# Performance work log

Measured on AMD Instinct MI355X. Metric: run time of the kernel, lower is better.

The kernel has to match this reference:

```python
import jax, jax.numpy as jnp
import numpy as np

N, E, G = 50000, 800000, 128          # nodes, edges, graphs in batch
DF, DE, DT = 128, 256, 18             # dim_features, dim_embedding, dim_target
NUM_LAYERS = 4


def setup_inputs() -> dict:
    key = jax.random.key(0)
    ks = jax.random.split(key, 32)
    inp = {}
    inp["x"] = jax.random.normal(ks[0], (N, DF), jnp.float32)
    inp["edge_index"] = jax.random.randint(ks[1], (2, E), 0, N, dtype=jnp.int64)
    inp["batch"] = jnp.sort(jax.random.randint(ks[2], (N,), 0, G, dtype=jnp.int64))
    i = 3
    for l in range(NUM_LAYERS):
        din = DF if l == 0 else DE
        inp[f"Wl{l}"] = jax.random.normal(ks[i], (din, DE), jnp.float32) * (din ** -0.5); i += 1
        inp[f"bl{l}"] = jnp.zeros((DE,), jnp.float32)
        inp[f"Wr{l}"] = jax.random.normal(ks[i], (din, DE), jnp.float32) * (din ** -0.5); i += 1
        inp[f"Wm{l}"] = jax.random.normal(ks[i], (DE, DE), jnp.float32) * (DE ** -0.5); i += 1
        inp[f"bm{l}"] = jnp.zeros((DE,), jnp.float32)
    inp["fc1_W"] = jax.random.normal(ks[i], (NUM_LAYERS * DE, DE), jnp.float32) * ((NUM_LAYERS * DE) ** -0.5); i += 1
    inp["fc1_b"] = jnp.zeros((DE,), jnp.float32)
    inp["fc2_W"] = jax.random.normal(ks[i], (DE, DT), jnp.float32) * (DE ** -0.5); i += 1
    inp["fc2_b"] = jnp.zeros((DT,), jnp.float32)
    return inp


def _seg_max(v, idx, n):
    # scatter-max; empty segments -> 0 (PyG scatter 'max' convention)
    m = jax.ops.segment_max(v, idx, num_segments=n)
    return jnp.where(jnp.isfinite(m), m, 0.0)


def reference(x, edge_index, batch,
              Wl0, bl0, Wr0, Wm0, bm0,
              Wl1, bl1, Wr1, Wm1, bm1,
              Wl2, bl2, Wr2, Wm2, bm2,
              Wl3, bl3, Wr3, Wm3, bm3,
              fc1_W, fc1_b, fc2_W, fc2_b):
    src, dst = edge_index[0], edge_index[1]
    params = [(Wl0, bl0, Wr0, Wm0, bm0), (Wl1, bl1, Wr1, Wm1, bm1),
              (Wl2, bl2, Wr2, Wm2, bm2), (Wl3, bl3, Wr3, Wm3, bm3)]
    h = x
    outs = []
    for Wl, bl, Wr, Wm, bm in params:
        # SAGEConv(aggr='max'): lin_l(max_j x_j) + lin_r(x_i)
        agg = _seg_max(h[src], dst, h.shape[0])       # [N, din] gather + scatter-max
        h = agg @ Wl + bl + h @ Wr                    # [N, DE]
        h = jax.nn.relu(h @ Wm + bm)                  # fc_max + relu
        outs.append(h)
    hc = jnp.concatenate(outs, axis=1)                # [N, 4*DE]
    g = _seg_max(hc, batch, G)                        # global_max_pool -> [G, 4*DE]
    last_layer = jax.nn.relu(g @ fc1_W + fc1_b)       # [G, DE]
    out = last_layer @ fc2_W + fc2_b                  # [G, DT] (dropout = identity at eval)
    return jax.nn.log_softmax(out, axis=1), out, last_layer
```

## Files before the change

### kernel.cpp

```cpp
#include <hip/hip_runtime.h>
#include <stdint.h>

#define NN 50000
#define EE 800000
#define GG 128
#define DF 128
#define DE 256
#define NB 196

typedef unsigned short u16;
typedef __bf16 bf16x8 __attribute__((ext_vector_type(8)));
typedef float f32x4 __attribute__((ext_vector_type(4)));
typedef short s16x8 __attribute__((ext_vector_type(8)));

__device__ __forceinline__ float bf2f(u16 u) {
  union { unsigned int i; float f; } x; x.i = ((unsigned int)u) << 16; return x.f;
}
__device__ __forceinline__ u16 f2bf(float f) {
  union { float f; unsigned int i; } x; x.f = f;
  unsigned int i = x.i;
  return (u16)((i + 0x7fffu + ((i >> 16) & 1u)) >> 16);
}

__device__ __forceinline__ void async16(const void* g, void* l) {
  __builtin_amdgcn_global_load_lds(
      (const __attribute__((address_space(1))) void*)g,
      (__attribute__((address_space(3))) void*)l,
      16, 0, 0);
}

__device__ __forceinline__ s16x8 vmax8(s16x8 a, s16x8 b) {
  return __builtin_elementwise_max(a, b);
}

__global__ void detect_kernel(const u16* __restrict__ xr,
                              const unsigned* __restrict__ ei_words,
                              int* __restrict__ flags, int* __restrict__ bucket_cnt) {
  int tid = threadIdx.x;
  if (blockIdx.x == 1) {
    if (tid < NB) bucket_cnt[tid] = 0;
    return;
  }
  __shared__ int red[2];
  if (tid < 2) red[tid] = 0;
  __syncthreads();
  int found = 0;
  for (int it = 0; it < 32; it++) {
    int i = it * 256 + tid;
    u16 a = xr[2 * i], b = xr[2 * i + 1];
    if (((a >> 7) & 0xFFu) == 0xFFu) found = 1;
    if (((b >> 7) & 0xFFu) == 0xFFu) found = 1;
  }
  if (__ballot(found)) { if ((tid & 63) == 0) atomicOr(&red[0], 1); }
  int nz = 0;
  if (tid < 128) {
    for (int j = 0; j < 4; j++) {
      unsigned w = ei_words[2 * (tid * 4 + j) + 1];
      if (w != 0u) nz = 1;
    }
  }
  if (__ballot(nz)) { if ((tid & 63) == 0) atomicOr(&red[1], 1); }
  __syncthreads();
  if (tid == 0) { flags[0] = red[0]; flags[1] = red[1]; }
}

__device__ __forceinline__ u16 ldw(const void* p, int idx, int f) {
  return f ? f2bf(((const float*)p)[idx]) : ((const u16*)p)[idx];
}

struct ConvSeg { const void* src; u16* dst; int start_blk; int n; };

struct PrepArgs {
  ConvSeg s[12]; int nseg; int conv_blocks;
  const void* x; u16* acat_x; u16* xk;
  const void* ei; const void* batch;
  int* src32; int* dst32; int* batch32; int* bucket_cnt;
};

__global__ void prep_all(PrepArgs A, const int* __restrict__ flags) {
  int f = flags[0];
  int tid = threadIdx.x;
  int b = blockIdx.x;

  if (b < A.conv_blocks) {
    for (int i = 0; i < A.nseg; i++) {
      int nb = (A.s[i].n + 255) >> 8;
      if (b >= A.s[i].start_blk && b < A.s[i].start_blk + nb) {
        int idx = ((b - A.s[i].start_blk) << 8) + tid;
        if (idx < A.s[i].n) A.s[i].dst[idx] = ldw(A.s[i].src, idx, f);
        return;
      }
    }
    return;
  }
  b -= A.conv_blocks;

  if (b < 25000) {
    int i = b * 256 + tid;
    int node = i >> 7, d = i & 127;
    u16 v = ldw(A.x, i, f);
    A.acat_x[(long)node * 512 + d] = v;
    short s = (short)v;
    A.xk[i] = (u16)(s ^ ((s >> 15) & 0x7FFF));
    return;
  }
  b -= 25000;

  __shared__ int h[NB];
  if (tid < NB) h[tid] = 0;
  __syncthreads();
  int i64 = (flags[1] == 0);
  int e0 = b * 2048;
  for (int j = 0; j < 8; j++) {
    int i = e0 + j * 256 + tid;
    if (i < EE) {
      int s, d;
      if (i64) {
        s = (int)((const long long*)A.ei)[i];
        d = (int)((const long long*)A.ei)[EE + i];
      } else {
        s = ((const int*)A.ei)[i];
        d = ((const int*)A.ei)[EE + i];
      }
      s = min(max(s, 0), NN - 1);
      d = min(max(d, 0), NN - 1);
      A.src32[i] = s;
      A.dst32[i] = d;
      atomicAdd(&h[d >> 8], 1);
    }
    if (i < NN) {
      int bv = i64 ? (int)((const long long*)A.batch)[i] : ((const int*)A.batch)[i];
      A.batch32[i] = min(max(bv, 0), GG - 1);
    }
  }
  __syncthreads();
  if (tid < NB) atomicAdd(&A.bucket_cnt[tid], h[tid]);
}

struct TransArgs {
  const void* Wl[4]; const void* Wr[4]; const void* Wm[4]; const void* fc1W;
  u16* WcatT[4]; u16* WmT[4]; u16* fc1WT;
};

__global__ __launch_bounds__(256) void transpose_w(TransArgs T, const int* __restrict__ flags) {
  int f = flags[0];
  __shared__ u16 tile[64][65];
  int b = blockIdx.x;
  const void* src; u16* dst; int kt, ntile, Kd; int krow_off = 0;
  if (b < 16) {
    kt = b >> 2; ntile = b & 3; Kd = 256;
    if (kt * 64 < 128) { src = T.Wl[0]; } else { src = T.Wr[0]; krow_off = 128; }
    dst = T.WcatT[0];
  } else if (b < 112) {
    int l = 1 + (b - 16) / 32; int t = (b - 16) % 32;
    kt = t >> 2; ntile = t & 3; Kd = 512;
    if (kt * 64 < 256) { src = T.Wl[l]; } else { src = T.Wr[l]; krow_off = 256; }
    dst = T.WcatT[l];
  } else if (b < 176) {
    int l = (b - 112) / 16; int t = (b - 112) % 16;
    kt = t >> 2; ntile = t & 3; Kd = 256;
    src = T.Wm[l]; dst = T.WmT[l];
  } else {
    int t = b - 176;
    kt = t >> 2; ntile = t & 3; Kd = 1024;
    src = T.fc1W; dst = T.fc1WT;
  }
  int cj = threadIdx.x & 63, rp = threadIdx.x >> 6;
#pragma unroll 4
  for (int p = 0; p < 16; p++) {
    int krow = kt * 64 + p * 4 + rp;
    tile[p * 4 + rp][cj] = ldw(src, (krow - krow_off) * 256 + ntile * 64 + cj, f);
  }
  __syncthreads();
#pragma unroll 4
  for (int p = 0; p < 16; p++) {
    int nrow = ntile * 64 + p * 4 + rp;
    dst[(long)nrow * Kd + kt * 64 + cj] = tile[cj][p * 4 + rp];
  }
}

__global__ void bucket_scan(const int* __restrict__ bucket_cnt, int* __restrict__ bucket_base,
                            int* __restrict__ bucket_cur,
                            const int* __restrict__ batch, int* __restrict__ gs) {
  __shared__ int sh[256];
  int tid = threadIdx.x;
  int x = (tid < NB) ? bucket_cnt[tid] : 0;
  sh[tid] = x;
  __syncthreads();
  for (int off = 1; off < 256; off <<= 1) {
    int v = (tid >= off) ? sh[tid - off] : 0;
    __syncthreads();
    sh[tid] += v;
    __syncthreads();
  }
  if (tid < NB) { bucket_base[tid] = sh[tid] - x; bucket_cur[tid] = sh[tid] - x; }
  if (tid == 0) bucket_base[NB] = EE;
  if (tid <= GG) {
    int g = tid, lo = 0, hi = NN;
    while (lo < hi) { int mid = (lo + hi) >> 1; if (batch[mid] < g) lo = mid + 1; else hi = mid; }
    gs[g] = lo;
  }
}

__global__ __launch_bounds__(256) void bucket_pass1(
    const int* __restrict__ src32, const int* __restrict__ dst32,
    int* __restrict__ bucket_cur, unsigned* __restrict__ bucket_buf) {
  __shared__ int lcnt[NB];
  __shared__ int lbase[NB];
  int tid = threadIdx.x, b = blockIdx.x;
  if (tid < NB) lcnt[tid] = 0;
  __syncthreads();
  int e0 = b * 2048;
  int lofs[8]; unsigned pk[8]; int bk[8];
#pragma unroll
  for (int j = 0; j < 8; j++) {
    int i = e0 + j * 256 + tid;
    if (i < EE) {
      int s = src32[i], d = dst32[i];
      bk[j] = d >> 8;
      pk[j] = ((unsigned)s << 8) | (unsigned)(d & 255);
      lofs[j] = atomicAdd(&lcnt[bk[j]], 1);
    } else bk[j] = -1;
  }
  __syncthreads();
  if (tid < NB) lbase[tid] = atomicAdd(&bucket_cur[tid], lcnt[tid]);
  __syncthreads();
#pragma unroll
  for (int j = 0; j < 8; j++)
    if (bk[j] >= 0)
      bucket_buf[lbase[bk[j]] + lofs[j]] = pk[j];
}

__global__ __launch_bounds__(256) void bucket_pass2(
    const unsigned* __restrict__ bucket_buf, const int* __restrict__ bucket_base,
    int* __restrict__ col_src, int* __restrict__ row_ptr) {
  __shared__ int cnt[256];
  __shared__ int sh[256];
  __shared__ int cur[256];
  int tid = threadIdx.x, b = blockIdx.x;
  int ebase = bucket_base[b], eend = bucket_base[b + 1];
  cnt[tid] = 0;
  __syncthreads();
  for (int e = ebase + tid; e < eend; e += 256)
    atomicAdd(&cnt[bucket_buf[e] & 255u], 1);
  __syncthreads();
  int x = cnt[tid];
  sh[tid] = x;
  __syncthreads();
  for (int off = 1; off < 256; off <<= 1) {
    int v = (tid >= off) ? sh[tid - off] : 0;
    __syncthreads();
    sh[tid] += v;
    __syncthreads();
  }
  int node = b * 256 + tid;
  if (node < NN) row_ptr[node + 1] = ebase + sh[tid];
  cur[tid] = ebase + sh[tid] - x;
  __syncthreads();
  for (int e = ebase + tid; e < eend; e += 256) {
    unsigned p = bucket_buf[e];
    int slot = atomicAdd(&cur[p & 255u], 1);
    col_src[slot] = (int)(p >> 8);
  }
  if (b == 0 && tid == 0) row_ptr[0] = 0;
}

template <int LPR, bool KEYED>
__global__ __launch_bounds__(256) void segmax_kernel(
    const u16* __restrict__ feat, int fstride,
    const int* __restrict__ row_ptr, const int* __restrict__ col_src,
    u16* __restrict__ agg_out, int ostride, int n) {
  constexpr int R = 64 / LPR;
  int node = blockIdx.x * 4 + (threadIdx.x >> 6);
  if (node >= n) return;
  int lane = threadIdx.x & 63;
  int sub = lane / LPR;
  int cp = lane % LPR;
  int beg = row_ptr[node], end = row_ptr[node + 1];
  s16x8 m = (s16x8)(short)(KEYED ? (short)0x807F : (short)0);
  const u16* fb = feat + cp * 8;

  int e = beg + sub;
  for (; e + 3 * R < end; e += 4 * R) {
    int s0 = col_src[e];
    int s1 = col_src[e + R];
    int s2 = col_src[e + 2 * R];
    int s3 = col_src[e + 3 * R];
    s16x8 v0 = *(const s16x8*)(fb + (long)s0 * fstride);
    s16x8 v1 = *(const s16x8*)(fb + (long)s1 * fstride);
    s16x8 v2 = *(const s16x8*)(fb + (long)s2 * fstride);
    s16x8 v3 = *(const s16x8*)(fb + (long)s3 * fstride);
    m = vmax8(m, vmax8(vmax8(v0, v1), vmax8(v2, v3)));
  }
  for (; e < end; e += R)
    m = vmax8(m, *(const s16x8*)(fb + (long)col_src[e] * fstride));

#pragma unroll
  for (int d = LPR; d < 64; d <<= 1) {
    union { s16x8 s; int i[4]; } t;
    t.s = m;
#pragma unroll
    for (int j = 0; j < 4; j++) t.i[j] = __shfl_xor(t.i[j], d);
    m = vmax8(m, t.s);
  }

  if (sub == 0) {
    if (KEYED) {
      if (beg == end) {
        m = (s16x8)(short)0;
      } else {
        s16x8 sp = (m >> 15) & (short)0x7FFF;
        m = m ^ sp;
      }
    }
    *(s16x8*)(agg_out + (long)node * ostride + cp * 8) = m;
  }
}

__global__ __launch_bounds__(512) void gemm256w(
    const u16* __restrict__ A, int lda, int K,
    const u16* __restrict__ BT,
    const u16* __restrict__ bias,
    u16* __restrict__ C, int ldc, int M, int relu_flag) {
  __shared__ u16 lsA[128 * 32];
  __shared__ u16 lsB[256 * 32];
  int tid = threadIdx.x;
  int lane = tid & 63, w = tid >> 6;
  int bm = blockIdx.x;
  int wm = (w & 1) << 6, wn = (w >> 1) << 6;
  int ln15 = lane & 15, quad = lane >> 4;

  f32x4 acc[4][4] = {};

  int r = tid >> 2;
  int c = (tid & 3) ^ (r & 3);
  const u16* gA = A + (long)min(bm * 128 + r, M - 1) * lda + c * 8;
  const u16* gB0 = BT + (long)r * K + c * 8;
  const u16* gB1 = BT + (long)(r + 128) * K + c * 8;
  u16* lA = lsA + w * 512;
  u16* lB0 = lsB + w * 512;
  u16* lB1 = lsB + 4096 + w * 512;
  int swz = (quad ^ (ln15 & 3)) << 3;

  for (int k0 = 0; k0 < K; k0 += 32) {
    async16(gA + k0, lA);
    async16(gB0 + k0, lB0);
    async16(gB1 + k0, lB1);
    __syncthreads();
    bf16x8 af[4], bfr[4];
#pragma unroll
    for (int t = 0; t < 4; t++) {
      af[t]  = *(const bf16x8*)(lsA + (wm + t * 16 + ln15) * 32 + swz);
      bfr[t] = *(const bf16x8*)(lsB + (wn + t * 16 + ln15) * 32 + swz);
    }
#pragma unroll
    for (int mt = 0; mt < 4; mt++)
#pragma unroll
      for (int nt = 0; nt < 4; nt++)
        acc[mt][nt] = __builtin_amdgcn_mfma_f32_16x16x32_bf16(af[mt], bfr[nt], acc[mt][nt], 0, 0, 0);
    __syncthreads();
  }

  float bv[4];
#pragma unroll
  for (int nt = 0; nt < 4; nt++)
    bv[nt] = bf2f(bias[wn + nt * 16 + ln15]);

#pragma unroll
  for (int mt = 0; mt < 4; mt++) {
    int row0 = bm * 128 + wm + mt * 16 + quad * 4;
#pragma unroll
    for (int rr = 0; rr < 4; rr++) {
      int row = row0 + rr;
      if (row < M) {
#pragma unroll
        for (int nt = 0; nt < 4; nt++) {
          float v = acc[mt][nt][rr] + bv[nt];
          if (relu_flag) v = fmaxf(v, 0.f);
          C[(long)row * ldc + wn + nt * 16 + ln15] = f2bf(v);
        }
      }
    }
  }
}

__global__ void pool_kernel(const u16* __restrict__ h, const int* __restrict__ gs,
                            u16* __restrict__ g_pool, int l) {
  int g = blockIdx.x;
  int chunk = threadIdx.x & 31;
  int rg = threadIdx.x >> 5;
  int beg = gs[g], end = gs[g + 1];
  s16x8 m = (s16x8)(short)0;
  const u16* hp = h + chunk * 8;
  for (int n = beg + rg; n < end; n += 32)
    m = vmax8(m, *(const s16x8*)(hp + (long)n * 512));
  __shared__ s16x8 red[32][32];
  red[rg][chunk] = m;
  __syncthreads();
  for (int s = 16; s >= 1; s >>= 1) {
    if (rg < s) red[rg][chunk] = vmax8(red[rg][chunk], red[rg + s][chunk]);
    __syncthreads();
  }
  if (rg == 0)
    *(s16x8*)(g_pool + g * 1024 + l * 256 + chunk * 8) = red[0][chunk];
}

__global__ __launch_bounds__(256) void fc1_gemm(
    const u16* __restrict__ A,
    const u16* __restrict__ BT,
    float* __restrict__ Cpart) {
  __shared__ u16 lsA[128 * 32];
  __shared__ u16 lsB[128 * 32];
  int tid = threadIdx.x;
  int lane = tid & 63, w = tid >> 6;
  int slice = blockIdx.x >> 1, bn = blockIdx.x & 1;
  int wm = (w & 1) << 6, wn = (w >> 1) << 6;
  int ln15 = lane & 15, quad = lane >> 4;

  f32x4 acc[4][4] = {};

  int cm = lane >> 2;
  int ck = (lane & 3) << 3;
  int kb = slice * 256;

  const u16* gA0 = A + (long)(w * 16 + cm) * 1024 + kb + ck;
  const u16* gA1 = A + (long)((w + 4) * 16 + cm) * 1024 + kb + ck;
  const u16* gB0 = BT + (long)(bn * 128 + w * 16 + cm) * 1024 + kb + ck;
  const u16* gB1 = BT + (long)(bn * 128 + (w + 4) * 16 + cm) * 1024 + kb + ck;
  u16* lA0 = lsA + w * 512;
  u16* lA1 = lsA + (w + 4) * 512;
  u16* lB0 = lsB + w * 512;
  u16* lB1 = lsB + (w + 4) * 512;

  for (int k0 = 0; k0 < 256; k0 += 32) {
    async16(gA0 + k0, lA0);
    async16(gA1 + k0, lA1);
    async16(gB0 + k0, lB0);
    async16(gB1 + k0, lB1);
    __syncthreads();
    bf16x8 af[4], bfr[4];
#pragma unroll
    for (int t = 0; t < 4; t++) {
      af[t]  = *(const bf16x8*)(lsA + (wm + t * 16 + ln15) * 32 + quad * 8);
      bfr[t] = *(const bf16x8*)(lsB + (wn + t * 16 + ln15) * 32 + quad * 8);
    }
#pragma unroll
    for (int mt = 0; mt < 4; mt++)
#pragma unroll
      for (int nt = 0; nt < 4; nt++)
        acc[mt][nt] = __builtin_amdgcn_mfma_f32_16x16x32_bf16(af[mt], bfr[nt], acc[mt][nt], 0, 0, 0);
    __syncthreads();
  }

  float* Cb = Cpart + slice * (GG * 256);
#pragma unroll
  for (int mt = 0; mt < 4; mt++) {
    int row0 = wm + mt * 16 + quad * 4;
#pragma unroll
    for (int r = 0; r < 4; r++)
#pragma unroll
      for (int nt = 0; nt < 4; nt++)
        Cb[(row0 + r) * 256 + bn * 128 + wn + nt * 16 + ln15] = acc[mt][nt][r];
  }
}

__global__ void fc2_head(const float* __restrict__ fc1part,
                         const u16* __restrict__ fc1b,
                         const u16* __restrict__ W,
                         const u16* __restrict__ b,
                         void* __restrict__ outbuf, const int* __restrict__ flags) {
  int g = blockIdx.x, t = threadIdx.x;
  __shared__ float lr[256];
  __shared__ float ps[144];
  __shared__ float sv[18];
  __shared__ float sred[2];
  float v = bf2f(fc1b[t]);
#pragma unroll
  for (int s = 0; s < 4; s++) v += fc1part[s * (GG * 256) + g * 256 + t];
  v = fmaxf(v, 0.f);
  lr[t] = v;
  if (flags[0]) ((float*)outbuf)[4608 + g * 256 + t] = v;
  else          ((u16*)outbuf)[4608 + g * 256 + t] = f2bf(v);
  __syncthreads();
  if (t < 144) {
    int o = t % 18, s = t / 18;
    float acc = 0.f;
    int k0 = s * 32;
#pragma unroll 8
    for (int k = k0; k < k0 + 32; k++)
      acc += lr[k] * bf2f(W[k * 18 + o]);
    ps[t] = acc;
  }
  __syncthreads();
  if (t < 18) {
    float acc = bf2f(b[t]);
#pragma unroll
    for (int s = 0; s < 8; s++) acc += ps[s * 18 + t];
    sv[t] = acc;
  }
  __syncthreads();
  if (t == 0) {
    float mx = sv[0];
    for (int i = 1; i < 18; i++) mx = fmaxf(mx, sv[i]);
    float s = 0.f;
    for (int i = 0; i < 18; i++) s += expf(sv[i] - mx);
    sred[0] = mx; sred[1] = logf(s);
  }
  __syncthreads();
  if (t < 18) {
    float raw = sv[t];
    float lsm = raw - sred[0] - sred[1];
    if (flags[0]) {
      ((float*)outbuf)[g * 18 + t] = lsm;
      ((float*)outbuf)[2304 + g * 18 + t] = raw;
    } else {
      ((u16*)outbuf)[g * 18 + t] = f2bf(lsm);
      ((u16*)outbuf)[2304 + g * 18 + t] = f2bf(raw);
    }
  }
}

extern "C" void kernel_launch(void* const* d_in, const int* in_sizes, int n_in,
                              void* d_out, int out_size, void* d_ws, size_t ws_size,
                              hipStream_t stream) {
  (void)in_sizes; (void)n_in; (void)out_size; (void)ws_size;
  const void* x = d_in[0];
  const void* ei = d_in[1];
  const void* batch = d_in[2];
  const void *Wl[4], *bl[4], *Wr[4], *Wm[4], *bm[4];
  for (int l = 0; l < 4; l++) {
    Wl[l] = d_in[3 + l * 5 + 0];
    bl[l] = d_in[3 + l * 5 + 1];
    Wr[l] = d_in[3 + l * 5 + 2];
    Wm[l] = d_in[3 + l * 5 + 3];
    bm[l] = d_in[3 + l * 5 + 4];
  }
  const void* fc1W = d_in[23];
  const void* fc1b = d_in[24];
  const void* fc2W = d_in[25];
  const void* fc2b = d_in[26];

  char* ws = (char*)d_ws;
  size_t off = 0;
  auto alloc = [&](size_t bytes) -> void* {
    void* p = ws + off;
    off = (off + bytes + 255) & ~(size_t)255;
    return p;
  };
  int* flags       = (int*)alloc(16);
  int* row_ptr     = (int*)alloc((NN + 1) * sizeof(int));
  int* bucket_cnt  = (int*)alloc(NB * sizeof(int));
  int* bucket_base = (int*)alloc((NB + 1) * sizeof(int));
  int* bucket_cur  = (int*)alloc(NB * sizeof(int));
  unsigned* bucket_buf = (unsigned*)alloc((size_t)EE * sizeof(unsigned));
  int* col_src = (int*)alloc((size_t)EE * sizeof(int));
  int* src32   = (int*)alloc((size_t)EE * sizeof(int));
  int* dst32   = (int*)alloc((size_t)EE * sizeof(int));
  int* batch32 = (int*)alloc(NN * sizeof(int));
  int* gs      = (int*)alloc((GG + 1) * sizeof(int));
  u16* WcatT[4]; for (int l = 0; l < 4; l++) WcatT[l] = (u16*)alloc(256 * 512 * 2);
  u16* WmT[4];   for (int l = 0; l < 4; l++) WmT[l]   = (u16*)alloc(256 * 256 * 2);
  u16* bl_bf[4]; for (int l = 0; l < 4; l++) bl_bf[l] = (u16*)alloc(256 * 2);
  u16* bm_bf[4]; for (int l = 0; l < 4; l++) bm_bf[l] = (u16*)alloc(256 * 2);
  u16* fc1WT   = (u16*)alloc(256 * 1024 * 2);
  u16* fc1b_bf = (u16*)alloc(256 * 2);
  u16* fc2W_bf = (u16*)alloc(256 * 18 * 2);
  u16* fc2b_bf = (u16*)alloc(18 * 2);
  u16* xk      = (u16*)alloc((size_t)NN * DF * 2);
  u16* Acat    = (u16*)alloc((size_t)NN * 512 * 2);
  u16* tmp     = (u16*)alloc((size_t)NN * 256 * 2);
  u16* gpool   = (u16*)alloc(GG * 1024 * 2);
  float* fc1part = (float*)alloc(4 * GG * 256 * sizeof(float));

  detect_kernel<<<2, 256, 0, stream>>>((const u16*)x, (const unsigned*)ei, flags, bucket_cnt);

  TransArgs TA;
  for (int l = 0; l < 4; l++) {
    TA.Wl[l] = Wl[l]; TA.Wr[l] = Wr[l]; TA.Wm[l] = Wm[l];
    TA.WcatT[l] = WcatT[l]; TA.WmT[l] = WmT[l];
  }
  TA.fc1W = fc1W; TA.fc1WT = fc1WT;
  transpose_w<<<240, 256, 0, stream>>>(TA, flags);

  PrepArgs PA;
  int blk = 0, si = 0;
  auto addseg = [&](const void* s, u16* d, int n) {
    PA.s[si].src = s; PA.s[si].dst = d; PA.s[si].start_blk = blk; PA.s[si].n = n;
    blk += (n + 255) / 256; si++;
  };
  addseg(fc2W, fc2W_bf, 256 * 18);
  for (int l = 0; l < 4; l++) addseg(bl[l], bl_bf[l], 256);
  for (int l = 0; l < 4; l++) addseg(bm[l], bm_bf[l], 256);
  addseg(fc1b, fc1b_bf, 256);
  addseg(fc2b, fc2b_bf, 18);
  PA.nseg = si; PA.conv_blocks = blk;
  PA.x = x; PA.acat_x = Acat + DF; PA.xk = xk;
  PA.ei = ei; PA.batch = batch;
  PA.src32 = src32; PA.dst32 = dst32; PA.batch32 = batch32; PA.bucket_cnt = bucket_cnt;
  prep_all<<<PA.conv_blocks + 25000 + 391, 256, 0, stream>>>(PA, flags);

  bucket_scan<<<1, 256, 0, stream>>>(bucket_cnt, bucket_base, bucket_cur, batch32, gs);
  bucket_pass1<<<391, 256, 0, stream>>>(src32, dst32, bucket_cur, bucket_buf);
  bucket_pass2<<<NB, 256, 0, stream>>>(bucket_buf, bucket_base, col_src, row_ptr);

  int segblocks = (NN + 3) / 4;
  int gemmgrid = (NN + 127) / 128;

  for (int l = 0; l < 4; l++) {
    if (l == 0) {
      segmax_kernel<16, true><<<segblocks, 256, 0, stream>>>(xk, DF, row_ptr, col_src,
                                                             Acat, 512, NN);
    } else {
      segmax_kernel<32, false><<<segblocks, 256, 0, stream>>>(Acat + 256, 512, row_ptr, col_src,
                                                              Acat, 512, NN);
    }
    int K = (l == 0) ? 256 : 512;
    gemm256w<<<gemmgrid, 512, 0, stream>>>(Acat, 512, K, WcatT[l], bl_bf[l], tmp, 256, NN, 0);
    gemm256w<<<gemmgrid, 512, 0, stream>>>(tmp, 256, 256, WmT[l], bm_bf[l], Acat + 256, 512, NN, 1);
    pool_kernel<<<GG, 1024, 0, stream>>>(Acat + 256, gs, gpool, l);
  }

  fc1_gemm<<<8, 256, 0, stream>>>(gpool, fc1WT, fc1part);
  fc2_head<<<GG, 256, 0, stream>>>(fc1part, fc1b_bf, fc2W_bf, fc2b_bf, d_out, flags);
}
```

Measured before the change: 560.6 us.

## Fuse per-layer SAGE linear and fc_max GEMMs into one kernel via LDS intermediate

```diff
diff --git a/kernel.cpp b/kernel.cpp
--- a/kernel.cpp
+++ b/kernel.cpp
@@ -7,6 +7,7 @@
 #define DF 128
 #define DE 256
 #define NB 196
+#define TSTR 264
 
 typedef unsigned short u16;
 typedef __bf16 bf16x8 __attribute__((ext_vector_type(8)));
@@ -317,40 +318,49 @@
   }
 }
 
-__global__ __launch_bounds__(512) void gemm256w(
+__global__ __launch_bounds__(256) void layer_fused(
     const u16* __restrict__ A, int lda, int K,
-    const u16* __restrict__ BT,
-    const u16* __restrict__ bias,
-    u16* __restrict__ C, int ldc, int M, int relu_flag) {
-  __shared__ u16 lsA[128 * 32];
+    const u16* __restrict__ B1T,
+    const u16* __restrict__ bias1,
+    const u16* __restrict__ B2T,
+    const u16* __restrict__ bias2,
+    u16* __restrict__ C, int ldc, int M) {
+  __shared__ u16 tmpT[64 * TSTR];
   __shared__ u16 lsB[256 * 32];
+  u16* lsA = tmpT;
   int tid = threadIdx.x;
   int lane = tid & 63, w = tid >> 6;
   int bm = blockIdx.x;
-  int wm = (w & 1) << 6, wn = (w >> 1) << 6;
+  int wn = w << 6;
   int ln15 = lane & 15, quad = lane >> 4;
 
   f32x4 acc[4][4] = {};
 
   int r = tid >> 2;
   int c = (tid & 3) ^ (r & 3);
-  const u16* gA = A + (long)min(bm * 128 + r, M - 1) * lda + c * 8;
-  const u16* gB0 = BT + (long)r * K + c * 8;
-  const u16* gB1 = BT + (long)(r + 128) * K + c * 8;
-  u16* lA = lsA + w * 512;
+  const u16* gA  = A + (long)min(bm * 64 + r, M - 1) * lda + c * 8;
+  const u16* g10 = B1T + (long)r * K + c * 8;
+  const u16* g11 = B1T + (long)(r + 64) * K + c * 8;
+  const u16* g12 = B1T + (long)(r + 128) * K + c * 8;
+  const u16* g13 = B1T + (long)(r + 192) * K + c * 8;
+  u16* lA  = lsA + w * 512;
   u16* lB0 = lsB + w * 512;
-  u16* lB1 = lsB + 4096 + w * 512;
+  u16* lB1 = lB0 + 2048;
+  u16* lB2 = lB0 + 4096;
+  u16* lB3 = lB0 + 6144;
   int swz = (quad ^ (ln15 & 3)) << 3;
 
   for (int k0 = 0; k0 < K; k0 += 32) {
     async16(gA + k0, lA);
-    async16(gB0 + k0, lB0);
-    async16(gB1 + k0, lB1);
+    async16(g10 + k0, lB0);
+    async16(g11 + k0, lB1);
+    async16(g12 + k0, lB2);
+    async16(g13 + k0, lB3);
     __syncthreads();
     bf16x8 af[4], bfr[4];
 #pragma unroll
     for (int t = 0; t < 4; t++) {
-      af[t]  = *(const bf16x8*)(lsA + (wm + t * 16 + ln15) * 32 + swz);
+      af[t]  = *(const bf16x8*)(lsA + (t * 16 + ln15) * 32 + swz);
       bfr[t] = *(const bf16x8*)(lsB + (wn + t * 16 + ln15) * 32 + swz);
     }
 #pragma unroll
@@ -361,22 +371,63 @@
     __syncthreads();
   }
 
-  float bv[4];
+  {
+    float bv1[4];
+#pragma unroll
+    for (int nt = 0; nt < 4; nt++)
+      bv1[nt] = bf2f(bias1[wn + nt * 16 + ln15]);
+#pragma unroll
+    for (int mt = 0; mt < 4; mt++) {
+      int row0 = mt * 16 + quad * 4;
+#pragma unroll
+      for (int rr = 0; rr < 4; rr++)
+#pragma unroll
+        for (int nt = 0; nt < 4; nt++)
+          tmpT[(row0 + rr) * TSTR + wn + nt * 16 + ln15] = f2bf(acc[mt][nt][rr] + bv1[nt]);
+    }
+  }
+
+  f32x4 acc2[4][4] = {};
+  const u16* g20 = B2T + (long)r * 256 + c * 8;
+  const u16* g21 = B2T + (long)(r + 64) * 256 + c * 8;
+  const u16* g22 = B2T + (long)(r + 128) * 256 + c * 8;
+  const u16* g23 = B2T + (long)(r + 192) * 256 + c * 8;
+
+  for (int k2 = 0; k2 < 256; k2 += 32) {
+    async16(g20 + k2, lB0);
+    async16(g21 + k2, lB1);
+    async16(g22 + k2, lB2);
+    async16(g23 + k2, lB3);
+    __syncthreads();
+    bf16x8 af[4], bfr[4];
+#pragma unroll
+    for (int t = 0; t < 4; t++) {
+      af[t]  = *(const bf16x8*)(tmpT + (t * 16 + ln15) * TSTR + k2 + quad * 8);
+      bfr[t] = *(const bf16x8*)(lsB + (wn + t * 16 + ln15) * 32 + swz);
+    }
+#pragma unroll
+    for (int mt = 0; mt < 4; mt++)
+#pragma unroll
+      for (int nt = 0; nt < 4; nt++)
+        acc2[mt][nt] = __builtin_amdgcn_mfma_f32_16x16x32_bf16(af[mt], bfr[nt], acc2[mt][nt], 0, 0, 0);
+    __syncthreads();
+  }
+
+  float bv2[4];
 #pragma unroll
   for (int nt = 0; nt < 4; nt++)
-    bv[nt] = bf2f(bias[wn + nt * 16 + ln15]);
+    bv2[nt] = bf2f(bias2[wn + nt * 16 + ln15]);
 
 #pragma unroll
   for (int mt = 0; mt < 4; mt++) {
-    int row0 = bm * 128 + wm + mt * 16 + quad * 4;
+    int row0 = bm * 64 + mt * 16 + quad * 4;
 #pragma unroll
     for (int rr = 0; rr < 4; rr++) {
       int row = row0 + rr;
       if (row < M) {
 #pragma unroll
         for (int nt = 0; nt < 4; nt++) {
-          float v = acc[mt][nt][rr] + bv[nt];
-          if (relu_flag) v = fmaxf(v, 0.f);
+          float v = fmaxf(acc2[mt][nt][rr] + bv2[nt], 0.f);
           C[(long)row * ldc + wn + nt * 16 + ln15] = f2bf(v);
         }
       }
@@ -568,7 +619,6 @@
   u16* fc2b_bf = (u16*)alloc(18 * 2);
   u16* xk      = (u16*)alloc((size_t)NN * DF * 2);
   u16* Acat    = (u16*)alloc((size_t)NN * 512 * 2);
-  u16* tmp     = (u16*)alloc((size_t)NN * 256 * 2);
   u16* gpool   = (u16*)alloc(GG * 1024 * 2);
   float* fc1part = (float*)alloc(4 * GG * 256 * sizeof(float));
 
@@ -604,7 +654,7 @@
   bucket_pass2<<<NB, 256, 0, stream>>>(bucket_buf, bucket_base, col_src, row_ptr);
 
   int segblocks = (NN + 3) / 4;
-  int gemmgrid = (NN + 127) / 128;
+  int fusedgrid = (NN + 63) / 64;
 
   for (int l = 0; l < 4; l++) {
     if (l == 0) {
@@ -615,8 +665,8 @@
                                                               Acat, 512, NN);
     }
     int K = (l == 0) ? 256 : 512;
-    gemm256w<<<gemmgrid, 512, 0, stream>>>(Acat, 512, K, WcatT[l], bl_bf[l], tmp, 256, NN, 0);
-    gemm256w<<<gemmgrid, 512, 0, stream>>>(tmp, 256, 256, WmT[l], bm_bf[l], Acat + 256, 512, NN, 1);
+    layer_fused<<<fusedgrid, 256, 0, stream>>>(Acat, 512, K, WcatT[l], bl_bf[l],
+                                               WmT[l], bm_bf[l], Acat + 256, 512, NN);
     pool_kernel<<<GG, 1024, 0, stream>>>(Acat + 256, gs, gpool, l);
   }
 
```

After: 579.7 us. +3.4%, slower.

## Shrink GEMM row tile to 64 with 4 waves and vectorize input prep

Applied to the files above, without the earlier changes.

```diff
diff --git a/kernel.cpp b/kernel.cpp
--- a/kernel.cpp
+++ b/kernel.cpp
@@ -95,16 +95,28 @@
   }
   b -= A.conv_blocks;
 
-  if (b < 25000) {
-    int i = b * 256 + tid;
+  if (b < 3125) {
+    int i = (b * 256 + tid) * 8;
     int node = i >> 7, d = i & 127;
-    u16 v = ldw(A.x, i, f);
-    A.acat_x[(long)node * 512 + d] = v;
-    short s = (short)v;
-    A.xk[i] = (u16)(s ^ ((s >> 15) & 0x7FFF));
+    union { u16 u[8]; uint4 v; } o, kx;
+    if (f) {
+      const float4* xp = (const float4*)((const float*)A.x + i);
+      float4 a = xp[0], q = xp[1];
+      o.u[0] = f2bf(a.x); o.u[1] = f2bf(a.y); o.u[2] = f2bf(a.z); o.u[3] = f2bf(a.w);
+      o.u[4] = f2bf(q.x); o.u[5] = f2bf(q.y); o.u[6] = f2bf(q.z); o.u[7] = f2bf(q.w);
+    } else {
+      o.v = *(const uint4*)((const u16*)A.x + i);
+    }
+#pragma unroll
+    for (int j = 0; j < 8; j++) {
+      short s = (short)o.u[j];
+      kx.u[j] = (u16)(s ^ ((s >> 15) & 0x7FFF));
+    }
+    *(uint4*)(A.acat_x + (long)node * 512 + d) = o.v;
+    *(uint4*)(A.xk + i) = kx.v;
     return;
   }
-  b -= 25000;
+  b -= 3125;
 
   __shared__ int h[NB];
   if (tid < NB) h[tid] = 0;
@@ -317,40 +329,46 @@
   }
 }
 
-__global__ __launch_bounds__(512) void gemm256w(
+__global__ __launch_bounds__(256) void gemm64(
     const u16* __restrict__ A, int lda, int K,
     const u16* __restrict__ BT,
     const u16* __restrict__ bias,
     u16* __restrict__ C, int ldc, int M, int relu_flag) {
-  __shared__ u16 lsA[128 * 32];
+  __shared__ u16 lsA[64 * 32];
   __shared__ u16 lsB[256 * 32];
   int tid = threadIdx.x;
   int lane = tid & 63, w = tid >> 6;
   int bm = blockIdx.x;
-  int wm = (w & 1) << 6, wn = (w >> 1) << 6;
+  int wn = w << 6;
   int ln15 = lane & 15, quad = lane >> 4;
 
   f32x4 acc[4][4] = {};
 
   int r = tid >> 2;
   int c = (tid & 3) ^ (r & 3);
-  const u16* gA = A + (long)min(bm * 128 + r, M - 1) * lda + c * 8;
-  const u16* gB0 = BT + (long)r * K + c * 8;
-  const u16* gB1 = BT + (long)(r + 128) * K + c * 8;
-  u16* lA = lsA + w * 512;
+  const u16* gA = A + (long)min(bm * 64 + r, M - 1) * lda + c * 8;
+  const u16* g0 = BT + (long)r * K + c * 8;
+  const u16* g1 = BT + (long)(r + 64) * K + c * 8;
+  const u16* g2 = BT + (long)(r + 128) * K + c * 8;
+  const u16* g3 = BT + (long)(r + 192) * K + c * 8;
+  u16* lA  = lsA + w * 512;
   u16* lB0 = lsB + w * 512;
-  u16* lB1 = lsB + 4096 + w * 512;
+  u16* lB1 = lB0 + 2048;
+  u16* lB2 = lB0 + 4096;
+  u16* lB3 = lB0 + 6144;
   int swz = (quad ^ (ln15 & 3)) << 3;
 
   for (int k0 = 0; k0 < K; k0 += 32) {
     async16(gA + k0, lA);
-    async16(gB0 + k0, lB0);
-    async16(gB1 + k0, lB1);
+    async16(g0 + k0, lB0);
+    async16(g1 + k0, lB1);
+    async16(g2 + k0, lB2);
+    async16(g3 + k0, lB3);
     __syncthreads();
     bf16x8 af[4], bfr[4];
 #pragma unroll
     for (int t = 0; t < 4; t++) {
-      af[t]  = *(const bf16x8*)(lsA + (wm + t * 16 + ln15) * 32 + swz);
+      af[t]  = *(const bf16x8*)(lsA + (t * 16 + ln15) * 32 + swz);
       bfr[t] = *(const bf16x8*)(lsB + (wn + t * 16 + ln15) * 32 + swz);
     }
 #pragma unroll
@@ -368,7 +386,7 @@
 
 #pragma unroll
   for (int mt = 0; mt < 4; mt++) {
-    int row0 = bm * 128 + wm + mt * 16 + quad * 4;
+    int row0 = bm * 64 + mt * 16 + quad * 4;
 #pragma unroll
     for (int rr = 0; rr < 4; rr++) {
       int row = row0 + rr;
@@ -597,14 +615,14 @@
   PA.x = x; PA.acat_x = Acat + DF; PA.xk = xk;
   PA.ei = ei; PA.batch = batch;
   PA.src32 = src32; PA.dst32 = dst32; PA.batch32 = batch32; PA.bucket_cnt = bucket_cnt;
-  prep_all<<<PA.conv_blocks + 25000 + 391, 256, 0, stream>>>(PA, flags);
+  prep_all<<<PA.conv_blocks + 3125 + 391, 256, 0, stream>>>(PA, flags);
 
   bucket_scan<<<1, 256, 0, stream>>>(bucket_cnt, bucket_base, bucket_cur, batch32, gs);
   bucket_pass1<<<391, 256, 0, stream>>>(src32, dst32, bucket_cur, bucket_buf);
   bucket_pass2<<<NB, 256, 0, stream>>>(bucket_buf, bucket_base, col_src, row_ptr);
 
   int segblocks = (NN + 3) / 4;
-  int gemmgrid = (NN + 127) / 128;
+  int gemmgrid = (NN + 63) / 64;
 
   for (int l = 0; l < 4; l++) {
     if (l == 0) {
@@ -615,8 +633,8 @@
                                                               Acat, 512, NN);
     }
     int K = (l == 0) ? 256 : 512;
-    gemm256w<<<gemmgrid, 512, 0, stream>>>(Acat, 512, K, WcatT[l], bl_bf[l], tmp, 256, NN, 0);
-    gemm256w<<<gemmgrid, 512, 0, stream>>>(tmp, 256, 256, WmT[l], bm_bf[l], Acat + 256, 512, NN, 1);
+    gemm64<<<gemmgrid, 256, 0, stream>>>(Acat, 512, K, WcatT[l], bl_bf[l], tmp, 256, NN, 0);
+    gemm64<<<gemmgrid, 256, 0, stream>>>(tmp, 256, 256, WmT[l], bm_bf[l], Acat + 256, 512, NN, 1);
     pool_kernel<<<GG, 1024, 0, stream>>>(Acat + 256, gs, gpool, l);
   }
 
```

After: 616.6 us. +10.0%, slower.
